# Kernel tuning notes

Hardware: AMD Instinct MI355X
Metric: run time of the kernel (lower is better)

Reference implementation:

```python
import jax, jax.numpy as jnp
import numpy as np

SCALE_BASE = 512.0
GAMMA = 0.96875


def _rotate_every_two(x):
    x1 = x[..., ::2]
    x2 = x[..., 1::2]
    return jnp.stack([-x2, x1], axis=-1).reshape(x.shape)


def _dup_interleave(m):
    # [L, d/2] -> [L, d], each column duplicated: (a,b) -> (a,a,b,b)
    return jnp.repeat(m, 2, axis=-1)


def _xpos(x, downscale=False):
    # x: [B, L, d]; offset = 0 (parallel form)
    B, L, d = x.shape
    half = d // 2
    pos = jnp.arange(L, dtype=x.dtype)
    # xpos per-channel scale base
    sv = (jnp.arange(0, d, 2, dtype=x.dtype) + 0.4 * d) / (1.4 * d)   # [d/2]
    scale = sv[None, :] ** (pos[:, None] / SCALE_BASE)                 # [L, d/2]
    if downscale:
        scale = 1.0 / scale
    inv_freq = 1.0 / (10000.0 ** (jnp.arange(half, dtype=x.dtype) / half))
    sinusoid = pos[:, None] * inv_freq[None, :]                        # [L, d/2]
    sin = _dup_interleave(jnp.sin(sinusoid) * scale)                   # [L, d]
    cos = _dup_interleave(jnp.cos(sinusoid) * scale)                   # [L, d]
    return x * cos[None] + _rotate_every_two(x) * sin[None]


def _get_D(seq_len, dtype):
    idx = jnp.arange(seq_len)
    diff = idx[:, None] - idx[None, :]                                 # n - m
    safe = jnp.where(diff >= 0, diff, 0).astype(dtype)
    return jnp.where(diff >= 0, GAMMA ** safe, jnp.zeros((), dtype))   # [L, L]


def setup_inputs() -> dict:
    key = jax.random.key(0)
    k1, k2, k3, k4 = jax.random.split(key, 4)
    B, L, H, D = 2, 4096, 1024, 64
    X = jax.random.normal(k1, (B, L, H), dtype=jnp.float32)
    W_Q = jax.random.normal(k2, (H, D), dtype=jnp.float32) / H
    W_K = jax.random.normal(k3, (H, D), dtype=jnp.float32) / H
    W_V = jax.random.normal(k4, (H, D), dtype=jnp.float32) / H
    return {"X": X, "W_Q": W_Q, "W_K": W_K, "W_V": W_V}


def reference(X, W_Q, W_K, W_V):
    L = X.shape[1]
    Dmask = _get_D(L, X.dtype)                     # [L, L]
    Q = _xpos(X @ W_Q)                             # [B, L, d]
    K = _xpos(X @ W_K, downscale=True)             # [B, L, d]
    V = X @ W_V                                    # [B, L, v]
    ret = jnp.einsum('bnd,bmd->bnm', Q, K) * Dmask[None]  # [B, L, L]
    return ret @ V                                 # [B, L, v]
```

## Files before the change

kernel.cpp:

```cpp
#include <hip/hip_runtime.h>
#include <math.h>

#define NB 2
#define LL 4096
#define HH 1024
#define DD 64
#define CHK 64
#define NCH 64
#define BLROWS (NB*LL)
#define NCHT (NB*NCH)
#define GAMMA 0.96875f

typedef _Float16 f16x8 __attribute__((ext_vector_type(8)));
typedef _Float16 f16x4 __attribute__((ext_vector_type(4)));
typedef float    f32x4 __attribute__((ext_vector_type(4)));

__global__ __launch_bounds__(256) void proj_mfma(
    const float* __restrict__ X, const float* __restrict__ WQ,
    const float* __restrict__ WK, const float* __restrict__ WV,
    _Float16* __restrict__ Qr, _Float16* __restrict__ Kf,
    _Float16* __restrict__ Vf)
{
    __shared__ __align__(16) _Float16 lds[12288];
    _Float16* Xh = lds;
    _Float16* Xl = lds + 2048;
    _Float16* Wh = lds + 4096;
    _Float16* Wl = lds + 8192;

    const int tid  = threadIdx.x;
    const int wv   = tid >> 6;
    const int lane = tid & 63;
    const int quad = lane >> 4;
    const int l15  = lane & 15;
    const int r0   = (blockIdx.x & 255) * 32;
    const int cb4  = (blockIdx.x >> 8) * 4;
    const int rt   = wv & 1;
    const int cp   = (wv >> 1) * 2;
    const float* Wm = (cb4 == 0) ? WQ : (cb4 == 4) ? WK : WV;

    const int xrow = tid >> 3;
    const int xk8  = (tid & 7) * 8;
    const int xslot = (((xrow >> 4) * 2 + (xk8 >> 5)) * 64 +
                       ((xk8 >> 3) & 3) * 16 + (xrow & 15)) * 8;
    int wd[2], wk[2];
#pragma unroll
    for (int i = 0; i < 2; ++i) {
        const int s = tid + i * 256;
        wd[i] = (s >> 7) * 16 + (s & 15);
        wk[i] = ((s >> 6) & 1) * 32 + ((s >> 4) & 3) * 8;
    }

    f32x4 acc[2];
    acc[0] = (f32x4){0.f, 0.f, 0.f, 0.f};
    acc[1] = (f32x4){0.f, 0.f, 0.f, 0.f};

    float4 pxa, pxb;
    float  pw[2][8];
    {
        const float* xp = &X[(size_t)(r0 + xrow) * HH + xk8];
        pxa = *(const float4*)&xp[0];
        pxb = *(const float4*)&xp[4];
#pragma unroll
        for (int i = 0; i < 2; ++i)
#pragma unroll
            for (int j = 0; j < 8; ++j)
                pw[i][j] = Wm[(size_t)(wk[i] + j) * DD + wd[i]];
    }

    for (int ch = 0; ch < 16; ++ch) {
        __syncthreads();
        {
            const float xv[8] = {pxa.x, pxa.y, pxa.z, pxa.w,
                                 pxb.x, pxb.y, pxb.z, pxb.w};
            f16x8 hv, lv;
#pragma unroll
            for (int e = 0; e < 8; ++e) {
                const _Float16 h = (_Float16)xv[e];
                hv[e] = h;
                lv[e] = (_Float16)(xv[e] - (float)h);
            }
            *(f16x8*)&Xh[xslot] = hv;
            *(f16x8*)&Xl[xslot] = lv;
#pragma unroll
            for (int i = 0; i < 2; ++i) {
                f16x8 whv, wlv;
#pragma unroll
                for (int j = 0; j < 8; ++j) {
                    const float x = pw[i][j] * 1024.f;
                    const _Float16 h = (_Float16)x;
                    whv[j] = h;
                    wlv[j] = (_Float16)(x - (float)h);
                }
                *(f16x8*)&Wh[(tid + i * 256) * 8] = whv;
                *(f16x8*)&Wl[(tid + i * 256) * 8] = wlv;
            }
        }
        __syncthreads();
        if (ch + 1 < 16) {
            const float* xp = &X[(size_t)(r0 + xrow) * HH + (ch + 1) * 64 + xk8];
            pxa = *(const float4*)&xp[0];
            pxb = *(const float4*)&xp[4];
            const int kb = (ch + 1) * 64;
#pragma unroll
            for (int i = 0; i < 2; ++i)
#pragma unroll
                for (int j = 0; j < 8; ++j)
                    pw[i][j] = Wm[(size_t)(kb + wk[i] + j) * DD + wd[i]];
        }
#pragma unroll
        for (int kt = 0; kt < 2; ++kt) {
            const f16x8 aH = *(const f16x8*)&Xh[((rt * 2 + kt) * 64 + lane) * 8];
            const f16x8 aL = *(const f16x8*)&Xl[((rt * 2 + kt) * 64 + lane) * 8];
#pragma unroll
            for (int cj = 0; cj < 2; ++cj) {
                const int ctl = cp + cj;
                const f16x8 bh = *(const f16x8*)&Wh[((ctl * 2 + kt) * 64 + lane) * 8];
                const f16x8 bl = *(const f16x8*)&Wl[((ctl * 2 + kt) * 64 + lane) * 8];
                acc[cj] = __builtin_amdgcn_mfma_f32_16x16x32_f16(aH, bh, acc[cj], 0, 0, 0);
                acc[cj] = __builtin_amdgcn_mfma_f32_16x16x32_f16(aH, bl, acc[cj], 0, 0, 0);
                acc[cj] = __builtin_amdgcn_mfma_f32_16x16x32_f16(aL, bh, acc[cj], 0, 0, 0);
            }
        }
    }

#pragma unroll
    for (int cj = 0; cj < 2; ++cj) {
        const int ctg = cb4 + cp + cj;
        const f32x4 v = acc[cj];
        const int col = ctg * 16 + l15;
        const int mat = ctg >> 2;
        const int d   = col & 63;
        if (mat < 2) {
            const int i2 = d >> 1;
            const float sv   = (2.f * (float)i2 + 25.6f) / 89.6f;
            const float l2sv = log2f(sv);
            const float ifr  = exp2f(-13.28771237954945f * ((float)i2 / 32.f));
            const float sgn  = (mat == 0) ? 1.f : -1.f;
#pragma unroll
            for (int r = 0; r < 4; ++r) {
                const int row = r0 + rt * 16 + quad * 4 + r;
                const float val = v[r] * (1.f / 1024.f);
                const float p = __shfl_xor(val, 1, 64);
                const float pf  = (float)(row & (LL - 1));
                const float pfs = (float)(row & 63);
                const float scl = exp2f(sgn * (pfs * (1.f / 512.f)) * l2sv);
                float s, c;
                sincosf(pf * ifr, &s, &c);
                s *= scl; c *= scl;
                const float o = ((col & 1) == 0) ? val * c - p * s
                                                 : val * c + p * s;
                if (mat == 0) {
                    Qr[(size_t)row * DD + d] = (_Float16)o;
                } else {
                    const int b = row >> 12, posb = row & 4095;
                    Kf[(((size_t)b * 8 + (d >> 3)) * 4096 + posb) * 8 + (d & 7)] =
                        (_Float16)o;
                }
            }
        } else {
            f16x4 vv;
#pragma unroll
            for (int r = 0; r < 4; ++r) vv[r] = (_Float16)(v[r] * (1.f / 1024.f));
            const int row0 = r0 + rt * 16 + quad * 4;
            const int b = row0 >> 12, posb = row0 & 4095;
            *(f16x4*)&Vf[(((size_t)b * 512 + (posb >> 3)) * 64 + d) * 8 + (posb & 7)] = vv;
        }
    }
}

__global__ __launch_bounds__(256) void chunk_out(
    const _Float16* __restrict__ Qr, const _Float16* __restrict__ Kf,
    const _Float16* __restrict__ Vf, float* __restrict__ out)
{
    __shared__ __align__(16) unsigned char smraw[38464];
    _Float16* Sb  = (_Float16*)smraw;
    _Float16* svp = (_Float16*)(smraw + 37120);
    float*    pwl = (float*)(smraw + 38144);

    const int tid   = threadIdx.x;
    const int bc    = blockIdx.x;
    const int chunk = bc >> 1;
    const int nh    = (bc & 1) * 32;
    const int w     = tid >> 6;
    const int lane  = tid & 63;
    const int quad  = lane >> 4;
    const int l15   = lane & 15;
    const int mt    = w >> 1;
    const int npair = (w & 1) * 2;
    const int cloc  = chunk & 63;
    const int bB    = chunk >> 6;
    const size_t rowbase = (size_t)chunk * CHK + nh;
    const float l2g = log2f(GAMMA);

    if (tid < 65) pwl[tid] = exp2f((float)tid * l2g);
#pragma unroll
    for (int e = 0; e < 2; ++e) {
        const int idx = tid + e * 256;
        const int dl  = (idx >> 6) + 1;
        const int dd  = idx & 63;
        const float sv = (2.f * (float)(dd >> 1) + 25.6f) / 89.6f;
        svp[idx] = (_Float16)exp2f(0.125f * (float)dl * log2f(sv));
    }

    f16x8 aQ[2];
#pragma unroll
    for (int ks = 0; ks < 2; ++ks)
        aQ[ks] = *(const f16x8*)&Qr[(rowbase + mt * 16 + l15) * DD +
                                    ks * 32 + quad * 8];
    __syncthreads();

    f32x4 sA[2] = {(f32x4){0.f,0.f,0.f,0.f}, (f32x4){0.f,0.f,0.f,0.f}};
#pragma unroll
    for (int nt = 0; nt < 2; ++nt) {
        const int posb = cloc * 64 + (npair + nt) * 16 + l15;
#pragma unroll
        for (int ks = 0; ks < 2; ++ks) {
            const f16x8 bK = *(const f16x8*)&Kf[(((size_t)bB * 8 + ks * 4 + quad)
                                                * 4096 + posb) * 8];
            sA[nt] = __builtin_amdgcn_mfma_f32_16x16x32_f16(aQ[ks], bK, sA[nt], 0, 0, 0);
        }
    }
#pragma unroll
    for (int nt = 0; nt < 2; ++nt) {
        const int m = (npair + nt) * 16 + l15;
#pragma unroll
        for (int r = 0; r < 4; ++r) {
            const int nl = mt * 16 + quad * 4 + r;
            const int n64 = nh + nl;
            const float val = (n64 >= m) ? sA[nt][r] * pwl[n64 - m] : 0.f;
            Sb[nl * 580 + m] = (_Float16)val;
        }
    }

    for (int jc = (w & 1); jc < 32; jc += 2) {
        const int dlt = 8 - (jc >> 2);
        const bool valid = (dlt <= cloc);
        const int mq = (jc * 16 + l15) & 63;
        const float gl = valid ? exp2f((float)(64 * dlt - mq) * l2g) : 0.f;
        const _Float16 glh = (_Float16)gl;
        const int cs = valid ? (chunk - dlt) : chunk;
        const int posb = (cs & 63) * 64 + mq;
        f32x4 sc4 = (f32x4){0.f, 0.f, 0.f, 0.f};
#pragma unroll
        for (int ks = 0; ks < 2; ++ks) {
            const f16x8 bk = *(const f16x8*)&Kf[(((size_t)bB * 8 + ks * 4 + quad)
                                                * 4096 + posb) * 8];
            const f16x8 sv8 = *(const f16x8*)&svp[(dlt - 1) * 64 + ks * 32 + quad * 8];
            f16x8 b2;
#pragma unroll
            for (int j = 0; j < 8; ++j) b2[j] = bk[j] * glh * sv8[j];
            sc4 = __builtin_amdgcn_mfma_f32_16x16x32_f16(aQ[ks], b2, sc4, 0, 0, 0);
        }
#pragma unroll
        for (int r = 0; r < 4; ++r) {
            const int nl = mt * 16 + quad * 4 + r;
            const int na = nh + nl;
            Sb[nl * 580 + 64 + jc * 16 + l15] = (_Float16)(sc4[r] * pwl[na]);
        }
    }
    __syncthreads();

    f32x4 oA[2] = {(f32x4){0.f,0.f,0.f,0.f}, (f32x4){0.f,0.f,0.f,0.f}};
    for (int ks5 = 0; ks5 < 18; ++ks5) {
        const f16x8 aS = *(const f16x8*)&Sb[(mt * 16 + l15) * 580 +
                                            ks5 * 32 + quad * 8];
        const int m0 = ks5 * 32 + quad * 8;
        int gr;
        if (ks5 < 2) {
            gr = chunk * 64 + m0;
        } else {
            const int mc = m0 - 64;
            int cs2 = chunk - 8 + (mc >> 6);
            if (cs2 < (chunk & ~63)) cs2 = chunk;
            gr = cs2 * 64 + (mc & 63);
        }
        const int b2 = gr >> 12, pb = gr & 4095;
        const size_t vb = ((size_t)b2 * 512 + (pb >> 3)) * 64;
#pragma unroll
        for (int t = 0; t < 2; ++t) {
            const int dp = (npair + t) * 16 + l15;
            const f16x8 bV = *(const f16x8*)&Vf[(vb + dp) * 8];
            oA[t] = __builtin_amdgcn_mfma_f32_16x16x32_f16(aS, bV, oA[t], 0, 0, 0);
        }
    }
#pragma unroll
    for (int t = 0; t < 2; ++t)
#pragma unroll
        for (int r = 0; r < 4; ++r)
            out[(rowbase + mt * 16 + quad * 4 + r) * DD +
                (npair + t) * 16 + l15] = oA[t][r];
}

extern "C" void kernel_launch(void* const* d_in, const int* in_sizes, int n_in,
                              void* d_out, int out_size, void* d_ws, size_t ws_size,
                              hipStream_t stream)
{
    const float* X  = (const float*)d_in[0];
    const float* WQ = (const float*)d_in[1];
    const float* WK = (const float*)d_in[2];
    const float* WV = (const float*)d_in[3];
    float* outp = (float*)d_out;

    _Float16* Qr = (_Float16*)d_ws;
    _Float16* Kf = Qr + (size_t)BLROWS * DD;
    _Float16* Vf = Kf + (size_t)BLROWS * DD;

    hipLaunchKernelGGL(proj_mfma, dim3(768), dim3(256), 0, stream,
                       X, WQ, WK, WV, Qr, Kf, Vf);
    hipLaunchKernelGGL(chunk_out, dim3(2 * NCHT), dim3(256), 0, stream,
                       Qr, Kf, Vf, outp);
}
```

Baseline: 113.3 us.

## Pre-split weights into fp16 hi/lo in MFMA layout and narrow chunk_out blocks

A new prep kernel converts W_Q/W_K/W_V once into fp16 high/low pairs already in the MFMA fragment layout. The projection kernel can then load them with vector loads instead of doing strided scalar fp32 gathers and per-block conversion. The chunk_out kernel now gives each block 16 query rows instead of 32 and launches 512 blocks, which raises parallelism and cuts LDS use, with a padded stride of 584. The cost is an extra kernel launch, extra workspace, and rereading K/V across more blocks.

```diff
diff --git a/kernel.cpp b/kernel.cpp
--- a/kernel.cpp
+++ b/kernel.cpp
@@ -15,11 +15,43 @@
 typedef _Float16 f16x4 __attribute__((ext_vector_type(4)));
 typedef float    f32x4 __attribute__((ext_vector_type(4)));
 
+#define WCH 12288
+#define SBS 584
+
+__global__ __launch_bounds__(256) void prep_w(
+    const float* __restrict__ WQ, const float* __restrict__ WK,
+    const float* __restrict__ WV, _Float16* __restrict__ Whg,
+    _Float16* __restrict__ Wlg)
+{
+    const unsigned t = blockIdx.x * 256 + threadIdx.x;
+    const unsigned kchunk = t / 1536u;
+    const unsigned s = t - kchunk * 1536u;
+    const int ct2  = s >> 6;
+    const int lane = s & 63;
+    const int n16  = ct2 >> 1;
+    const int kt   = ct2 & 1;
+    const int quad = lane >> 4;
+    const int n    = n16 * 16 + (lane & 15);
+    const int k0   = (int)kchunk * 64 + kt * 32 + quad * 8;
+    const int m    = n >> 6;
+    const int d    = n & 63;
+    const float* Wm = (m == 0) ? WQ : (m == 1) ? WK : WV;
+    f16x8 hv, lv;
+#pragma unroll
+    for (int j = 0; j < 8; ++j) {
+        const float x = Wm[(size_t)(k0 + j) * DD + d] * 1024.f;
+        const _Float16 h = (_Float16)x;
+        hv[j] = h;
+        lv[j] = (_Float16)(x - (float)h);
+    }
+    *(f16x8*)&Whg[(size_t)t * 8] = hv;
+    *(f16x8*)&Wlg[(size_t)t * 8] = lv;
+}
+
 __global__ __launch_bounds__(256) void proj_mfma(
-    const float* __restrict__ X, const float* __restrict__ WQ,
-    const float* __restrict__ WK, const float* __restrict__ WV,
-    _Float16* __restrict__ Qr, _Float16* __restrict__ Kf,
-    _Float16* __restrict__ Vf)
+    const float* __restrict__ X, const _Float16* __restrict__ Whg,
+    const _Float16* __restrict__ Wlg, _Float16* __restrict__ Qr,
+    _Float16* __restrict__ Kf, _Float16* __restrict__ Vf)
 {
     __shared__ __align__(16) _Float16 lds[12288];
     _Float16* Xh = lds;
@@ -36,35 +68,30 @@
     const int cb4  = (blockIdx.x >> 8) * 4;
     const int rt   = wv & 1;
     const int cp   = (wv >> 1) * 2;
-    const float* Wm = (cb4 == 0) ? WQ : (cb4 == 4) ? WK : WV;
 
     const int xrow = tid >> 3;
     const int xk8  = (tid & 7) * 8;
     const int xslot = (((xrow >> 4) * 2 + (xk8 >> 5)) * 64 +
                        ((xk8 >> 3) & 3) * 16 + (xrow & 15)) * 8;
-    int wd[2], wk[2];
-#pragma unroll
-    for (int i = 0; i < 2; ++i) {
-        const int s = tid + i * 256;
-        wd[i] = (s >> 7) * 16 + (s & 15);
-        wk[i] = ((s >> 6) & 1) * 32 + ((s >> 4) & 3) * 8;
-    }
 
     f32x4 acc[2];
     acc[0] = (f32x4){0.f, 0.f, 0.f, 0.f};
     acc[1] = (f32x4){0.f, 0.f, 0.f, 0.f};
 
     float4 pxa, pxb;
-    float  pw[2][8];
+    f16x8  pwh[2], pwl2[2];
     {
         const float* xp = &X[(size_t)(r0 + xrow) * HH + xk8];
         pxa = *(const float4*)&xp[0];
         pxb = *(const float4*)&xp[4];
 #pragma unroll
-        for (int i = 0; i < 2; ++i)
-#pragma unroll
-            for (int j = 0; j < 8; ++j)
-                pw[i][j] = Wm[(size_t)(wk[i] + j) * DD + wd[i]];
+        for (int i = 0; i < 2; ++i) {
+            const int s = tid + i * 256;
+            const int ctl = s >> 7, kt = (s >> 6) & 1, ln = s & 63;
+            const size_t off = (size_t)(((cb4 + ctl) * 2 + kt) * 64 + ln) * 8;
+            pwh[i]  = *(const f16x8*)&Whg[off];
+            pwl2[i] = *(const f16x8*)&Wlg[off];
+        }
     }
 
     for (int ch = 0; ch < 16; ++ch) {
@@ -83,16 +110,8 @@
             *(f16x8*)&Xl[xslot] = lv;
 #pragma unroll
             for (int i = 0; i < 2; ++i) {
-                f16x8 whv, wlv;
-#pragma unroll
-                for (int j = 0; j < 8; ++j) {
-                    const float x = pw[i][j] * 1024.f;
-                    const _Float16 h = (_Float16)x;
-                    whv[j] = h;
-                    wlv[j] = (_Float16)(x - (float)h);
-                }
-                *(f16x8*)&Wh[(tid + i * 256) * 8] = whv;
-                *(f16x8*)&Wl[(tid + i * 256) * 8] = wlv;
+                *(f16x8*)&Wh[(tid + i * 256) * 8] = pwh[i];
+                *(f16x8*)&Wl[(tid + i * 256) * 8] = pwl2[i];
             }
         }
         __syncthreads();
@@ -100,12 +119,16 @@
             const float* xp = &X[(size_t)(r0 + xrow) * HH + (ch + 1) * 64 + xk8];
             pxa = *(const float4*)&xp[0];
             pxb = *(const float4*)&xp[4];
-            const int kb = (ch + 1) * 64;
-#pragma unroll
-            for (int i = 0; i < 2; ++i)
-#pragma unroll
-                for (int j = 0; j < 8; ++j)
-                    pw[i][j] = Wm[(size_t)(kb + wk[i] + j) * DD + wd[i]];
+            const size_t cb = (size_t)(ch + 1) * WCH;
+#pragma unroll
+            for (int i = 0; i < 2; ++i) {
+                const int s = tid + i * 256;
+                const int ctl = s >> 7, kt = (s >> 6) & 1, ln = s & 63;
+                const size_t off = cb +
+                    (size_t)(((cb4 + ctl) * 2 + kt) * 64 + ln) * 8;
+                pwh[i]  = *(const f16x8*)&Whg[off];
+                pwl2[i] = *(const f16x8*)&Wlg[off];
+            }
         }
 #pragma unroll
         for (int kt = 0; kt < 2; ++kt) {
@@ -172,24 +195,22 @@
     const _Float16* __restrict__ Qr, const _Float16* __restrict__ Kf,
     const _Float16* __restrict__ Vf, float* __restrict__ out)
 {
-    __shared__ __align__(16) unsigned char smraw[38464];
+    __shared__ __align__(16) unsigned char smraw[20032];
     _Float16* Sb  = (_Float16*)smraw;
-    _Float16* svp = (_Float16*)(smraw + 37120);
-    float*    pwl = (float*)(smraw + 38144);
+    _Float16* svp = (_Float16*)(smraw + 18688);
+    float*    pwl = (float*)(smraw + 19712);
 
     const int tid   = threadIdx.x;
     const int bc    = blockIdx.x;
-    const int chunk = bc >> 1;
-    const int nh    = (bc & 1) * 32;
+    const int chunk = bc >> 2;
+    const int qt    = bc & 3;
     const int w     = tid >> 6;
     const int lane  = tid & 63;
     const int quad  = lane >> 4;
     const int l15   = lane & 15;
-    const int mt    = w >> 1;
-    const int npair = (w & 1) * 2;
     const int cloc  = chunk & 63;
     const int bB    = chunk >> 6;
-    const size_t rowbase = (size_t)chunk * CHK + nh;
+    const size_t rowbase = (size_t)chunk * CHK + qt * 16;
     const float l2g = log2f(GAMMA);
 
     if (tid < 65) pwl[tid] = exp2f((float)tid * l2g);
@@ -205,34 +226,29 @@
     f16x8 aQ[2];
 #pragma unroll
     for (int ks = 0; ks < 2; ++ks)
-        aQ[ks] = *(const f16x8*)&Qr[(rowbase + mt * 16 + l15) * DD +
-                                    ks * 32 + quad * 8];
+        aQ[ks] = *(const f16x8*)&Qr[(rowbase + l15) * DD + ks * 32 + quad * 8];
     __syncthreads();
 
-    f32x4 sA[2] = {(f32x4){0.f,0.f,0.f,0.f}, (f32x4){0.f,0.f,0.f,0.f}};
-#pragma unroll
-    for (int nt = 0; nt < 2; ++nt) {
-        const int posb = cloc * 64 + (npair + nt) * 16 + l15;
+    {
+        const int posb = cloc * 64 + w * 16 + l15;
+        f32x4 sA = (f32x4){0.f, 0.f, 0.f, 0.f};
 #pragma unroll
         for (int ks = 0; ks < 2; ++ks) {
             const f16x8 bK = *(const f16x8*)&Kf[(((size_t)bB * 8 + ks * 4 + quad)
                                                 * 4096 + posb) * 8];
-            sA[nt] = __builtin_amdgcn_mfma_f32_16x16x32_f16(aQ[ks], bK, sA[nt], 0, 0, 0);
-        }
-    }
-#pragma unroll
-    for (int nt = 0; nt < 2; ++nt) {
-        const int m = (npair + nt) * 16 + l15;
+            sA = __builtin_amdgcn_mfma_f32_16x16x32_f16(aQ[ks], bK, sA, 0, 0, 0);
+        }
+        const int m = w * 16 + l15;
 #pragma unroll
         for (int r = 0; r < 4; ++r) {
-            const int nl = mt * 16 + quad * 4 + r;
-            const int n64 = nh + nl;
-            const float val = (n64 >= m) ? sA[nt][r] * pwl[n64 - m] : 0.f;
-            Sb[nl * 580 + m] = (_Float16)val;
-        }
-    }
-
-    for (int jc = (w & 1); jc < 32; jc += 2) {
+            const int nl = quad * 4 + r;
+            const int n64 = qt * 16 + nl;
+            const float val = (n64 >= m) ? sA[r] * pwl[n64 - m] : 0.f;
+            Sb[nl * SBS + m] = (_Float16)val;
+        }
+    }
+
+    for (int jc = w; jc < 32; jc += 4) {
         const int dlt = 8 - (jc >> 2);
         const bool valid = (dlt <= cloc);
         const int mq = (jc * 16 + l15) & 63;
@@ -253,17 +269,17 @@
         }
 #pragma unroll
         for (int r = 0; r < 4; ++r) {
-            const int nl = mt * 16 + quad * 4 + r;
-            const int na = nh + nl;
-            Sb[nl * 580 + 64 + jc * 16 + l15] = (_Float16)(sc4[r] * pwl[na]);
+            const int nl = quad * 4 + r;
+            const int na = qt * 16 + nl;
+            Sb[nl * SBS + 64 + jc * 16 + l15] = (_Float16)(sc4[r] * pwl[na]);
         }
     }
     __syncthreads();
 
-    f32x4 oA[2] = {(f32x4){0.f,0.f,0.f,0.f}, (f32x4){0.f,0.f,0.f,0.f}};
+    f32x4 oA = (f32x4){0.f, 0.f, 0.f, 0.f};
+    const int dp = w * 16 + l15;
     for (int ks5 = 0; ks5 < 18; ++ks5) {
-        const f16x8 aS = *(const f16x8*)&Sb[(mt * 16 + l15) * 580 +
-                                            ks5 * 32 + quad * 8];
+        const f16x8 aS = *(const f16x8*)&Sb[l15 * SBS + ks5 * 32 + quad * 8];
         const int m0 = ks5 * 32 + quad * 8;
         int gr;
         if (ks5 < 2) {
@@ -276,19 +292,12 @@
         }
         const int b2 = gr >> 12, pb = gr & 4095;
         const size_t vb = ((size_t)b2 * 512 + (pb >> 3)) * 64;
-#pragma unroll
-        for (int t = 0; t < 2; ++t) {
-            const int dp = (npair + t) * 16 + l15;
-            const f16x8 bV = *(const f16x8*)&Vf[(vb + dp) * 8];
-            oA[t] = __builtin_amdgcn_mfma_f32_16x16x32_f16(aS, bV, oA[t], 0, 0, 0);
-        }
-    }
-#pragma unroll
-    for (int t = 0; t < 2; ++t)
-#pragma unroll
-        for (int r = 0; r < 4; ++r)
-            out[(rowbase + mt * 16 + quad * 4 + r) * DD +
-                (npair + t) * 16 + l15] = oA[t][r];
+        const f16x8 bV = *(const f16x8*)&Vf[(vb + dp) * 8];
+        oA = __builtin_amdgcn_mfma_f32_16x16x32_f16(aS, bV, oA, 0, 0, 0);
+    }
+#pragma unroll
+    for (int r = 0; r < 4; ++r)
+        out[(rowbase + quad * 4 + r) * DD + dp] = oA[r];
 }
 
 extern "C" void kernel_launch(void* const* d_in, const int* in_sizes, int n_in,
@@ -301,12 +310,16 @@
     const float* WV = (const float*)d_in[3];
     float* outp = (float*)d_out;
 
-    _Float16* Qr = (_Float16*)d_ws;
-    _Float16* Kf = Qr + (size_t)BLROWS * DD;
-    _Float16* Vf = Kf + (size_t)BLROWS * DD;
-
+    _Float16* Whg = (_Float16*)d_ws;
+    _Float16* Wlg = Whg + 196608;
+    _Float16* Qr  = Wlg + 196608;
+    _Float16* Kf  = Qr + (size_t)BLROWS * DD;
+    _Float16* Vf  = Kf + (size_t)BLROWS * DD;
+
+    hipLaunchKernelGGL(prep_w, dim3(96), dim3(256), 0, stream,
+                       WQ, WK, WV, Whg, Wlg);
     hipLaunchKernelGGL(proj_mfma, dim3(768), dim3(256), 0, stream,
-                       X, WQ, WK, WV, Qr, Kf, Vf);
-    hipLaunchKernelGGL(chunk_out, dim3(2 * NCHT), dim3(256), 0, stream,
+                       X, Whg, Wlg, Qr, Kf, Vf);
+    hipLaunchKernelGGL(chunk_out, dim3(512), dim3(256), 0, stream,
                        Qr, Kf, Vf, outp);
 }
```

New measurement: 109.6 us. 3.3% less time.
